# Performance work log

Measured on AMD Instinct MI355X. Metric: run time of the kernel, lower is better.

Reference implementation:

```python
import jax, jax.numpy as jnp
import numpy as np

NEG_SLOPE = 0.2
EPS = 1e-5


def gatv2_conv(x, src, dst, Wl, Wr, att, bias, n_nodes):
    # x: [N, F_in]; Wl, Wr: [F_in, H*C]; att: [H, C]; bias: [C]
    H, C = att.shape
    xl = (x @ Wl).reshape(n_nodes, H, C)
    xr = (x @ Wr).reshape(n_nodes, H, C)
    # edge-wise GATv2 score: att . leaky_relu(xl[src] + xr[dst])
    xls = xl[src]                                   # [E, H, C]
    e = jax.nn.leaky_relu(xls + xr[dst], negative_slope=NEG_SLOPE)
    score = jnp.einsum('ehc,hc->eh', e, att)        # [E, H]
    # segment softmax over incoming edges of each dst node
    m = jax.ops.segment_max(score, dst, num_segments=n_nodes)
    expv = jnp.exp(score - m[dst])
    denom = jax.ops.segment_sum(expv, dst, num_segments=n_nodes)
    alpha = expv / denom[dst]                       # [E, H]
    out = jax.ops.segment_sum(xls * alpha[:, :, None], dst, num_segments=n_nodes)  # [N, H, C]
    return out.mean(axis=1) + bias                  # concat=False -> mean heads


def batchnorm(x, gamma, beta):
    mu = x.mean(axis=0)
    var = x.var(axis=0)
    return (x - mu) * jax.lax.rsqrt(var + EPS) * gamma + beta


def setup_inputs() -> dict:
    key = jax.random.key(0)
    ks = jax.random.split(key, 16)
    N, E = 50000, 400000
    F_in, Hd, H, Z = 32, 64, 4, 64

    def glorot(k, shape):
        fan_in, fan_out = shape[0], shape[-1]
        s = float(np.sqrt(6.0 / (fan_in + fan_out)))
        return jax.random.uniform(k, shape, jnp.float32, -s, s)

    return {
        'x': jax.random.normal(ks[0], (N, F_in), jnp.float32),
        'edge_index': jax.random.randint(ks[1], (2, E), 0, N, jnp.int64),
        'l': jax.random.uniform(ks[2], (N,), jnp.float32),
        'Wl1': glorot(ks[3], (F_in, H * Hd)),
        'Wr1': glorot(ks[4], (F_in, H * Hd)),
        'att1': glorot(ks[5], (H, Hd)),
        'b1': jnp.zeros((Hd,), jnp.float32),
        'g1': jnp.ones((Hd,), jnp.float32),
        'be1': jnp.zeros((Hd,), jnp.float32),
        'Wl2': glorot(ks[6], (Hd + 1, H * Hd)),
        'Wr2': glorot(ks[7], (Hd + 1, H * Hd)),
        'att2': glorot(ks[8], (H, Hd)),
        'b2': jnp.zeros((Hd,), jnp.float32),
        'g2': jnp.ones((Hd,), jnp.float32),
        'be2': jnp.zeros((Hd,), jnp.float32),
        'Wlin': glorot(ks[9], (Hd, 2 * Z)),
        'blin': jnp.zeros((2 * Z,), jnp.float32),
    }


def reference(x, edge_index, l, Wl1, Wr1, att1, b1, g1, be1,
              Wl2, Wr2, att2, b2, g2, be2, Wlin, blin):
    N = x.shape[0]
    loop = jnp.arange(N, dtype=edge_index.dtype)
    src = jnp.concatenate([edge_index[0], loop])  # add self-loops (PyG default)
    dst = jnp.concatenate([edge_index[1], loop])

    h = gatv2_conv(x, src, dst, Wl1, Wr1, att1, b1, N)
    h = jax.nn.relu(batchnorm(h, g1, be1))
    h = jnp.concatenate([h, l[:, None]], axis=-1)
    h = gatv2_conv(h, src, dst, Wl2, Wr2, att2, b2, N)
    h = jax.nn.relu(batchnorm(h, g2, be2))
    h = h @ Wlin + blin
    return h.mean(axis=0)  # [2*z_dim]
```

## Files before the change

### kernel.cpp

```cpp
#include <hip/hip_runtime.h>
#include <hip/hip_bf16.h>

typedef __hip_bfloat16 bf16;
typedef unsigned short u16;
typedef unsigned char u8;

#define NEG 0.2f
#define BN_EPS 1e-5f
#define SLOTS 64

typedef __attribute__((ext_vector_type(8))) short bfrag;
typedef __attribute__((ext_vector_type(4))) float ffrag;
typedef __attribute__((ext_vector_type(2))) float f32x2;

__device__ __forceinline__ float u2f(u16 u) { return __uint_as_float(((unsigned)u) << 16); }
__device__ __forceinline__ float lo2f(unsigned u) { return __uint_as_float(u << 16); }
__device__ __forceinline__ float hi2f(unsigned u) { return __uint_as_float(u & 0xffff0000u); }
__device__ __forceinline__ u16 f2b(float f) { bf16 t = __float2bfloat16(f); return *(u16*)&t; }
__device__ __forceinline__ float leaky(float x) { return fmaxf(x, NEG * x); }

__device__ __forceinline__ void prep_body(const float* __restrict__ Wl,
                                          const float* __restrict__ Wr,
                                          u16* __restrict__ Wbf, int K, int idx) {
    const int l = idx & 63, n = (idx >> 6) & 31, s = idx >> 11;
    const int col = n * 16 + (l & 15);
    const int kbase = s * 32 + ((l >> 4) << 3);
    const float* __restrict__ W = (col < 256) ? (Wl + col) : (Wr + col - 256);
    u16 v[8];
    #pragma unroll
    for (int j = 0; j < 8; ++j) {
        const int k = kbase + j;
        v[j] = (k < K) ? f2b(W[(size_t)k * 256]) : (u16)0;
    }
    ushort4* d = reinterpret_cast<ushort4*>(Wbf + (size_t)idx * 8);
    d[0] = make_ushort4(v[0], v[1], v[2], v[3]);
    d[1] = make_ushort4(v[4], v[5], v[6], v[7]);
}

__global__ __launch_bounds__(256) void k_misc(
    const float* __restrict__ Wl1, const float* __restrict__ Wr1,
    const float* __restrict__ Wl2, const float* __restrict__ Wr2,
    u16* __restrict__ WbfA, u16* __restrict__ WbfB,
    const int* __restrict__ src, const int* __restrict__ dst,
    int* __restrict__ deg, int* __restrict__ csr_off, int E) {
    const int b = blockIdx.x;
    if (b < 8) {
        prep_body(Wl1, Wr1, WbfA, 32, b * 256 + threadIdx.x);
    } else if (b < 32) {
        prep_body(Wl2, Wr2, WbfB, 65, (b - 8) * 256 + threadIdx.x);
    } else {
        for (int e = (b - 32) * 256 + (int)threadIdx.x; e < E; e += 1024 * 256) {
            const int d = dst[e];
            const int slot = atomicAdd(&deg[d], 1);
            if (slot < SLOTS) csr_off[d * SLOTS + slot] = src[e] * 256;
        }
    }
}

template <int KSTEPS, int STAGE, int SAW>
__device__ __forceinline__ void gemm_body(
    int bid,
    const float* __restrict__ Xf,
    const u16* __restrict__ hagg,
    const float* __restrict__ sums, const float* __restrict__ sumsq,
    const float* __restrict__ g, const float* __restrict__ be,
    const float* __restrict__ lf,
    const u16* __restrict__ Wbf,
    u8* __restrict__ xl, u8* __restrict__ xr, int N) {

    __shared__ u16 sA[32 * SAW];
    __shared__ u8 sC[32 * 512];
    __shared__ float ssc[64], ssh[64];

    const int tid = threadIdx.x;
    const int row0 = bid * 32;

    if (STAGE == 1) {
        if (tid < 64) {
            const float invN = 1.0f / (float)N;
            const float mu = sums[tid] * invN;
            const float var = sumsq[tid] * invN - mu * mu;
            const float sc = rsqrtf(var + BN_EPS) * g[tid];
            ssc[tid] = sc;
            ssh[tid] = be[tid] - mu * sc;
        }
        __syncthreads();
        for (int idx = tid; idx < 32 * 12; idx += 256) {
            const int r = idx / 12, c0 = (idx % 12) * 8;
            const int rr = row0 + r;
            u16 o[8] = {0, 0, 0, 0, 0, 0, 0, 0};
            if (rr < N) {
                if (c0 < 64) {
                    const uint4 hv = *reinterpret_cast<const uint4*>(hagg + (size_t)rr * 64 + c0);
                    const float f[8] = {lo2f(hv.x), hi2f(hv.x), lo2f(hv.y), hi2f(hv.y),
                                        lo2f(hv.z), hi2f(hv.z), lo2f(hv.w), hi2f(hv.w)};
                    #pragma unroll
                    for (int j = 0; j < 8; ++j)
                        o[j] = f2b(fmaxf(0.f, f[j] * ssc[c0 + j] + ssh[c0 + j]));
                } else if (c0 == 64) {
                    o[0] = f2b(lf[rr]);
                }
            }
            ushort4* d = reinterpret_cast<ushort4*>(&sA[r * SAW + c0]);
            d[0] = make_ushort4(o[0], o[1], o[2], o[3]);
            d[1] = make_ushort4(o[4], o[5], o[6], o[7]);
        }
    } else {
        for (int idx = tid; idx < 32 * 8; idx += 256) {
            const int r = idx >> 3, c4 = (idx & 7) * 4;
            const int rr = row0 + r;
            float4 v = make_float4(0.f, 0.f, 0.f, 0.f);
            if (rr < N) v = *reinterpret_cast<const float4*>(Xf + (size_t)rr * 32 + c4);
            *reinterpret_cast<ushort4*>(&sA[r * SAW + c4]) =
                make_ushort4(f2b(v.x), f2b(v.y), f2b(v.z), f2b(v.w));
        }
    }
    __syncthreads();

    const int w = tid >> 6, l = tid & 63;
    ffrag acc[2][8];
    #pragma unroll
    for (int m = 0; m < 2; ++m)
        #pragma unroll
        for (int n = 0; n < 8; ++n) acc[m][n] = ffrag{0.f, 0.f, 0.f, 0.f};

    #pragma unroll
    for (int s = 0; s < KSTEPS; ++s) {
        bfrag bf[8];
        #pragma unroll
        for (int n = 0; n < 8; ++n) {
            const int ntile = w * 8 + n;
            bf[n] = *reinterpret_cast<const bfrag*>(Wbf + ((size_t)(s * 32 + ntile) * 64 + l) * 8);
        }
        bfrag af[2];
        #pragma unroll
        for (int m = 0; m < 2; ++m) {
            const int off = (m * 16 + (l & 15)) * SAW + s * 32 + ((l >> 4) << 3);
            af[m] = *reinterpret_cast<const bfrag*>(&sA[off]);
        }
        #pragma unroll
        for (int n = 0; n < 8; ++n) {
            acc[0][n] = __builtin_amdgcn_mfma_f32_16x16x32_bf16(af[0], bf[n], acc[0][n], 0, 0, 0);
            acc[1][n] = __builtin_amdgcn_mfma_f32_16x16x32_bf16(af[1], bf[n], acc[1][n], 0, 0, 0);
        }
    }

    #pragma unroll
    for (int m = 0; m < 2; ++m)
        #pragma unroll
        for (int n = 0; n < 8; ++n) {
            const int col = w * 128 + n * 16 + (l & 15);
            const int rbase = m * 16 + ((l >> 4) << 2);
            unsigned w01 = __builtin_amdgcn_cvt_pk_fp8_f32(acc[m][n][0], acc[m][n][1], 0u, false);
            unsigned w23 = __builtin_amdgcn_cvt_pk_fp8_f32(acc[m][n][2], acc[m][n][3], 0u, false);
            sC[(rbase + 0) * 512 + col] = (u8)(w01 & 0xff);
            sC[(rbase + 1) * 512 + col] = (u8)((w01 >> 8) & 0xff);
            sC[(rbase + 2) * 512 + col] = (u8)(w23 & 0xff);
            sC[(rbase + 3) * 512 + col] = (u8)((w23 >> 8) & 0xff);
        }
    __syncthreads();

    for (int idx = tid; idx < 32 * 32; idx += 256) {
        const int r = idx >> 5, c16 = (idx & 31) * 16;
        const int rr = row0 + r;
        if (rr >= N) continue;
        const uint4 v = *reinterpret_cast<const uint4*>(&sC[r * 512 + c16]);
        if (c16 < 256)
            *reinterpret_cast<uint4*>(xl + (size_t)rr * 256 + c16) = v;
        else
            *reinterpret_cast<uint4*>(xr + (size_t)rr * 256 + (c16 - 256)) = v;
    }
}

__global__ __launch_bounds__(256) void k_gemm1(
    const float* __restrict__ Xf, const u16* __restrict__ WbfA,
    u8* __restrict__ xl, u8* __restrict__ xr, int N) {
    gemm_body<1, 0, 40>(blockIdx.x, Xf, nullptr, nullptr, nullptr, nullptr, nullptr,
                        nullptr, WbfA, xl, xr, N);
}

__global__ __launch_bounds__(256) void k_gemm2(
    const u16* __restrict__ hagg,
    const float* __restrict__ sums, const float* __restrict__ sumsq,
    const float* __restrict__ g, const float* __restrict__ be,
    const float* __restrict__ lf, const u16* __restrict__ WbfB,
    u8* __restrict__ xl, u8* __restrict__ xr, int N) {
    gemm_body<3, 1, 104>(blockIdx.x, nullptr, hagg, sums, sumsq, g, be, lf, WbfB, xl, xr, N);
}

__global__ __launch_bounds__(256) void gat_fused(
    const u8* __restrict__ xl, const u8* __restrict__ xr,
    const int* __restrict__ csr_off, const int* __restrict__ deg,
    const float* __restrict__ att,
    u16* __restrict__ hagg, int N) {
    const int tid = threadIdx.x;
    const int wv = tid >> 6, lane = tid & 63;
    const int id = blockIdx.x * 4 + wv;
    if (id >= N) return;
    const int half = lane >> 5, hl = lane & 31;

    const float4 av0 = *reinterpret_cast<const float4*>(att + hl * 8);
    const float4 av1 = *reinterpret_cast<const float4*>(att + hl * 8 + 4);
    const char* xlb = (const char*)xl;
    const unsigned selfOff = (unsigned)id * 256u;
    const unsigned laneOff = (unsigned)hl * 8u;

    const uint2 bu = *reinterpret_cast<const uint2*>((const char*)xr + selfOff + laneOff);
    const f32x2 bu01 = __builtin_amdgcn_cvt_pk_f32_fp8(bu.x, false);
    const f32x2 bu23 = __builtin_amdgcn_cvt_pk_f32_fp8(bu.x, true);
    const f32x2 bu45 = __builtin_amdgcn_cvt_pk_f32_fp8(bu.y, false);
    const f32x2 bu67 = __builtin_amdgcn_cvt_pk_f32_fp8(bu.y, true);
    const float b0 = bu01.x, b1 = bu01.y, b2 = bu23.x, b3 = bu23.y;
    const float b4 = bu45.x, b5 = bu45.y, b6 = bu67.x, b7 = bu67.y;

    const int L = min(deg[id], SLOTS);

    unsigned idxA = selfOff;
    if (lane < L) idxA = (unsigned)csr_off[id * SLOTS + lane];

    auto offv = [&](int vi) -> unsigned {
        const unsigned o = (unsigned)__shfl((int)idxA, vi - 1);
        return (vi == 0) ? selfOff : o;
    };
    auto ldrow = [&](int vi) -> uint2 {
        return *reinterpret_cast<const uint2*>(xlb + (size_t)(offv(vi) + laneOff));
    };

    float ax0 = 0.f, ax1 = 0.f, ax2 = 0.f, ax3 = 0.f;
    float ax4 = 0.f, ax5 = 0.f, ax6 = 0.f, ax7 = 0.f;
    float denom = 0.f;

    uint2 A = ldrow(half);
    uint2 B = ldrow(2 + half);

    #define PROC(a, vi)                                                         \
    {                                                                           \
        const f32x2 u01 = __builtin_amdgcn_cvt_pk_f32_fp8((a).x, false);        \
        const f32x2 u23 = __builtin_amdgcn_cvt_pk_f32_fp8((a).x, true);         \
        const f32x2 u45 = __builtin_amdgcn_cvt_pk_f32_fp8((a).y, false);        \
        const f32x2 u67 = __builtin_amdgcn_cvt_pk_f32_fp8((a).y, true);         \
        const float x0 = u01.x, x1 = u01.y, x2 = u23.x, x3 = u23.y;             \
        const float x4 = u45.x, x5 = u45.y, x6 = u67.x, x7 = u67.y;             \
        float p = av0.x * leaky(x0 + b0) + av0.y * leaky(x1 + b1)               \
                + av0.z * leaky(x2 + b2) + av0.w * leaky(x3 + b3)               \
                + av1.x * leaky(x4 + b4) + av1.y * leaky(x5 + b5)               \
                + av1.z * leaky(x6 + b6) + av1.w * leaky(x7 + b7);              \
        p += __shfl_xor(p, 1);                                                  \
        p += __shfl_xor(p, 2);                                                  \
        p += __shfl_xor(p, 4);                                                  \
        const float ev = ((vi) <= L) ? __expf(p) : 0.f;                         \
        denom += ev;                                                            \
        ax0 += ev * x0; ax1 += ev * x1; ax2 += ev * x2; ax3 += ev * x3;         \
        ax4 += ev * x4; ax5 += ev * x5; ax6 += ev * x6; ax7 += ev * x7;         \
    }

    for (int ib = 0; ib <= L; ib += 4) {
        uint2 An = A, Bn = B;
        if (ib + 4 <= L) An = ldrow(ib + 4 + half);
        if (ib + 6 <= L) Bn = ldrow(ib + 6 + half);
        PROC(A, ib + half)
        PROC(B, ib + 2 + half)
        A = An; B = Bn;
    }
    #undef PROC

    denom += __shfl_xor(denom, 32);
    const float s = 0.25f / denom;
    float r0 = ax0 * s, r1 = ax1 * s, r2 = ax2 * s, r3 = ax3 * s;
    float r4 = ax4 * s, r5 = ax5 * s, r6 = ax6 * s, r7 = ax7 * s;

    #define RED(r) r += __shfl_xor(r, 8); r += __shfl_xor(r, 16); r += __shfl_xor(r, 32);
    RED(r0) RED(r1) RED(r2) RED(r3) RED(r4) RED(r5) RED(r6) RED(r7)
    #undef RED

    if (lane < 8) {
        union { u16 h[8]; uint4 v; } pk;
        pk.h[0] = f2b(r0); pk.h[1] = f2b(r1); pk.h[2] = f2b(r2); pk.h[3] = f2b(r3);
        pk.h[4] = f2b(r4); pk.h[5] = f2b(r5); pk.h[6] = f2b(r6); pk.h[7] = f2b(r7);
        *reinterpret_cast<uint4*>(hagg + (size_t)id * 64 + lane * 8) = pk.v;
    }
}

__global__ __launch_bounds__(256) void bn_stats(const u16* __restrict__ hagg,
                                                float* __restrict__ sums,
                                                float* __restrict__ sumsq, int N) {
    __shared__ float bsum[64], bsq[64];
    const int tid = threadIdx.x;
    if (tid < 64) { bsum[tid] = 0.f; bsq[tid] = 0.f; }
    __syncthreads();
    const int r0 = tid >> 3, cg = tid & 7;
    float s[8] = {0, 0, 0, 0, 0, 0, 0, 0}, q[8] = {0, 0, 0, 0, 0, 0, 0, 0};
    for (int n = blockIdx.x * 32 + r0; n < N; n += gridDim.x * 32) {
        const uint4 v = *reinterpret_cast<const uint4*>(hagg + (size_t)n * 64 + cg * 8);
        const float f[8] = {lo2f(v.x), hi2f(v.x), lo2f(v.y), hi2f(v.y),
                            lo2f(v.z), hi2f(v.z), lo2f(v.w), hi2f(v.w)};
        #pragma unroll
        for (int j = 0; j < 8; ++j) { s[j] += f[j]; q[j] += f[j] * f[j]; }
    }
    #pragma unroll
    for (int j = 0; j < 8; ++j) {
        atomicAdd(&bsum[cg * 8 + j], s[j]);
        atomicAdd(&bsq[cg * 8 + j], q[j]);
    }
    __syncthreads();
    if (tid < 64) {
        atomicAdd(&sums[tid], bsum[tid]);
        atomicAdd(&sumsq[tid], bsq[tid]);
    }
}

__global__ __launch_bounds__(256) void bnz_final(
    const u16* __restrict__ hagg,
    const float* __restrict__ sums, const float* __restrict__ sumsq,
    const float* __restrict__ g, const float* __restrict__ be,
    const float* __restrict__ Wlin, const float* __restrict__ blin,
    float* __restrict__ zbar, int* __restrict__ counter,
    float* __restrict__ out, int N) {
    __shared__ float ls[4][64];
    __shared__ float zb[64];
    __shared__ int lastFlag;
    const int tid = threadIdx.x;
    const int c = tid & 63, r = tid >> 6;
    const float invN = 1.0f / (float)N;
    const float mu = sums[c] * invN;
    const float var = sumsq[c] * invN - mu * mu;
    const float sc = rsqrtf(var + BN_EPS) * g[c];
    const float sh = be[c] - mu * sc;
    float s = 0.f;
    for (int n = blockIdx.x * 4 + r; n < N; n += gridDim.x * 4)
        s += fmaxf(0.f, u2f(hagg[(size_t)n * 64 + c]) * sc + sh);
    ls[r][c] = s;
    __syncthreads();
    if (tid < 64) {
        atomicAdd(&zbar[tid], ls[0][tid] + ls[1][tid] + ls[2][tid] + ls[3][tid]);
        __threadfence();
    }
    __syncthreads();
    if (tid == 0) lastFlag = (atomicAdd(counter, 1) == (int)gridDim.x - 1) ? 1 : 0;
    __syncthreads();
    if (lastFlag) {
        if (tid < 64) zb[tid] = atomicAdd(&zbar[tid], 0.0f);
        __syncthreads();
        if (tid < 128) {
            float acc = blin[tid];
            #pragma unroll 4
            for (int k = 0; k < 64; ++k) acc += (zb[k] * invN) * Wlin[(size_t)k * 128 + tid];
            out[tid] = acc;
        }
    }
}

static inline char* align16(char* p) {
    return (char*)(((uintptr_t)p + 15) & ~(uintptr_t)15);
}

extern "C" void kernel_launch(void* const* d_in, const int* in_sizes, int n_in,
                              void* d_out, int out_size, void* d_ws, size_t ws_size,
                              hipStream_t stream) {
    const float* x    = (const float*)d_in[0];
    const int*   ei   = (const int*)d_in[1];
    const float* l    = (const float*)d_in[2];
    const float* Wl1  = (const float*)d_in[3];
    const float* Wr1  = (const float*)d_in[4];
    const float* att1 = (const float*)d_in[5];
    const float* g1   = (const float*)d_in[7];
    const float* be1  = (const float*)d_in[8];
    const float* Wl2  = (const float*)d_in[9];
    const float* Wr2  = (const float*)d_in[10];
    const float* att2 = (const float*)d_in[11];
    const float* g2   = (const float*)d_in[13];
    const float* be2  = (const float*)d_in[14];
    const float* Wlin = (const float*)d_in[15];
    const float* blin = (const float*)d_in[16];
    float* out = (float*)d_out;

    const int N = in_sizes[2];
    const int E = in_sizes[1] / 2;
    const int* src = ei;
    const int* dst = ei + E;

    char* p = (char*)d_ws;
    u8* xl = (u8*)p;            p += (size_t)N * 256 * sizeof(u8);
    u8* xr = (u8*)p;            p += (size_t)N * 256 * sizeof(u8);
    u16* hagg = (u16*)p;        p += (size_t)N * 64 * sizeof(u16);  p = align16(p);
    u16* WbfA = (u16*)p;        p += (size_t)2048 * 8 * sizeof(u16);
    u16* WbfB = (u16*)p;        p += (size_t)6144 * 8 * sizeof(u16);
    int* csr_off = (int*)p;     p += (size_t)N * SLOTS * sizeof(int);  p = align16(p);
    char* zero0 = p;
    int* deg = (int*)p;         p += (size_t)N * sizeof(int);
    int* scalars = (int*)p;
    float* sums1 = (float*)p;   p += 64 * sizeof(float);
    float* sumsq1 = (float*)p;  p += 64 * sizeof(float);
    float* sums2 = (float*)p;   p += 64 * sizeof(float);
    float* sumsq2 = (float*)p;  p += 64 * sizeof(float);
    float* zbar = (float*)p;    p += 64 * sizeof(float);
    int* counter = (int*)p;     p += 192 * sizeof(int);
    const size_t zbytes = (size_t)(p - zero0);
    (void)scalars;

    const int gemmBlocks = (N + 31) / 32;
    const int nodeBlocks = (N + 3) / 4;

    hipMemsetAsync(zero0, 0, zbytes, stream);
    k_misc<<<32 + 1024, 256, 0, stream>>>(Wl1, Wr1, Wl2, Wr2, WbfA, WbfB,
                                          src, dst, deg, csr_off, E);
    k_gemm1<<<gemmBlocks, 256, 0, stream>>>(x, WbfA, xl, xr, N);
    gat_fused<<<nodeBlocks, 256, 0, stream>>>(xl, xr, csr_off, deg, att1, hagg, N);
    bn_stats<<<256, 256, 0, stream>>>(hagg, sums1, sumsq1, N);
    k_gemm2<<<gemmBlocks, 256, 0, stream>>>(hagg, sums1, sumsq1, g1, be1, l, WbfB, xl, xr, N);
    gat_fused<<<nodeBlocks, 256, 0, stream>>>(xl, xr, csr_off, deg, att2, hagg, N);
    bn_stats<<<256, 256, 0, stream>>>(hagg, sums2, sumsq2, N);
    bnz_final<<<256, 256, 0, stream>>>(hagg, sums2, sumsq2, g2, be2, Wlin, blin,
                                       zbar, counter, out, N);
}
```

Before: 188.2 us.

## Overlap edge scatter with first GEMM and pack GAT math into float2 ops

Moves the edge-to-CSR atomic scatter out of the weight-prep kernel and into extra blocks of the first GEMM launch, so the scatter runs alongside the projection GEMM and the small prep kernel stays short. It also rewrites the per-edge leaky-relu, attention dot product and accumulation in gat_fused using 2-wide float vectors, so the compiler can emit packed FP32 instructions. The packed form changes the summation order of the attention dot product slightly. The GEMM blocks now share the GPU with atomic-heavy scatter blocks, which may contend for memory bandwidth.

```diff
diff --git a/kernel.cpp b/kernel.cpp
--- a/kernel.cpp
+++ b/kernel.cpp
@@ -17,7 +17,6 @@
 __device__ __forceinline__ float lo2f(unsigned u) { return __uint_as_float(u << 16); }
 __device__ __forceinline__ float hi2f(unsigned u) { return __uint_as_float(u & 0xffff0000u); }
 __device__ __forceinline__ u16 f2b(float f) { bf16 t = __float2bfloat16(f); return *(u16*)&t; }
-__device__ __forceinline__ float leaky(float x) { return fmaxf(x, NEG * x); }
 
 __device__ __forceinline__ void prep_body(const float* __restrict__ Wl,
                                           const float* __restrict__ Wr,
@@ -37,24 +36,13 @@
     d[1] = make_ushort4(v[4], v[5], v[6], v[7]);
 }
 
-__global__ __launch_bounds__(256) void k_misc(
+__global__ __launch_bounds__(256) void k_prep(
     const float* __restrict__ Wl1, const float* __restrict__ Wr1,
     const float* __restrict__ Wl2, const float* __restrict__ Wr2,
-    u16* __restrict__ WbfA, u16* __restrict__ WbfB,
-    const int* __restrict__ src, const int* __restrict__ dst,
-    int* __restrict__ deg, int* __restrict__ csr_off, int E) {
+    u16* __restrict__ WbfA, u16* __restrict__ WbfB) {
     const int b = blockIdx.x;
-    if (b < 8) {
-        prep_body(Wl1, Wr1, WbfA, 32, b * 256 + threadIdx.x);
-    } else if (b < 32) {
-        prep_body(Wl2, Wr2, WbfB, 65, (b - 8) * 256 + threadIdx.x);
-    } else {
-        for (int e = (b - 32) * 256 + (int)threadIdx.x; e < E; e += 1024 * 256) {
-            const int d = dst[e];
-            const int slot = atomicAdd(&deg[d], 1);
-            if (slot < SLOTS) csr_off[d * SLOTS + slot] = src[e] * 256;
-        }
-    }
+    if (b < 8) prep_body(Wl1, Wr1, WbfA, 32, b * 256 + threadIdx.x);
+    else       prep_body(Wl2, Wr2, WbfB, 65, (b - 8) * 256 + threadIdx.x);
 }
 
 template <int KSTEPS, int STAGE, int SAW>
@@ -172,11 +160,22 @@
     }
 }
 
-__global__ __launch_bounds__(256) void k_gemm1(
+__global__ __launch_bounds__(256) void k_gemm1_scatter(
     const float* __restrict__ Xf, const u16* __restrict__ WbfA,
-    u8* __restrict__ xl, u8* __restrict__ xr, int N) {
-    gemm_body<1, 0, 40>(blockIdx.x, Xf, nullptr, nullptr, nullptr, nullptr, nullptr,
-                        nullptr, WbfA, xl, xr, N);
+    u8* __restrict__ xl, u8* __restrict__ xr, int N, int gemmBlocks,
+    const int* __restrict__ src, const int* __restrict__ dst,
+    int* __restrict__ deg, int* __restrict__ csr_off, int E) {
+    if ((int)blockIdx.x < gemmBlocks) {
+        gemm_body<1, 0, 40>(blockIdx.x, Xf, nullptr, nullptr, nullptr, nullptr, nullptr,
+                            nullptr, WbfA, xl, xr, N);
+    } else {
+        for (int e = ((int)blockIdx.x - gemmBlocks) * 256 + (int)threadIdx.x; e < E;
+             e += 1024 * 256) {
+            const int d = dst[e];
+            const int slot = atomicAdd(&deg[d], 1);
+            if (slot < SLOTS) csr_off[d * SLOTS + slot] = src[e] * 256;
+        }
+    }
 }
 
 __global__ __launch_bounds__(256) void k_gemm2(
@@ -199,19 +198,20 @@
     if (id >= N) return;
     const int half = lane >> 5, hl = lane & 31;
 
-    const float4 av0 = *reinterpret_cast<const float4*>(att + hl * 8);
-    const float4 av1 = *reinterpret_cast<const float4*>(att + hl * 8 + 4);
+    const f32x2 av01 = *reinterpret_cast<const f32x2*>(att + hl * 8);
+    const f32x2 av23 = *reinterpret_cast<const f32x2*>(att + hl * 8 + 2);
+    const f32x2 av45 = *reinterpret_cast<const f32x2*>(att + hl * 8 + 4);
+    const f32x2 av67 = *reinterpret_cast<const f32x2*>(att + hl * 8 + 6);
     const char* xlb = (const char*)xl;
     const unsigned selfOff = (unsigned)id * 256u;
     const unsigned laneOff = (unsigned)hl * 8u;
+    const f32x2 negv = {NEG, NEG};
 
     const uint2 bu = *reinterpret_cast<const uint2*>((const char*)xr + selfOff + laneOff);
-    const f32x2 bu01 = __builtin_amdgcn_cvt_pk_f32_fp8(bu.x, false);
-    const f32x2 bu23 = __builtin_amdgcn_cvt_pk_f32_fp8(bu.x, true);
-    const f32x2 bu45 = __builtin_amdgcn_cvt_pk_f32_fp8(bu.y, false);
-    const f32x2 bu67 = __builtin_amdgcn_cvt_pk_f32_fp8(bu.y, true);
-    const float b0 = bu01.x, b1 = bu01.y, b2 = bu23.x, b3 = bu23.y;
-    const float b4 = bu45.x, b5 = bu45.y, b6 = bu67.x, b7 = bu67.y;
+    const f32x2 b01 = __builtin_amdgcn_cvt_pk_f32_fp8(bu.x, false);
+    const f32x2 b23 = __builtin_amdgcn_cvt_pk_f32_fp8(bu.x, true);
+    const f32x2 b45 = __builtin_amdgcn_cvt_pk_f32_fp8(bu.y, false);
+    const f32x2 b67 = __builtin_amdgcn_cvt_pk_f32_fp8(bu.y, true);
 
     const int L = min(deg[id], SLOTS);
 
@@ -226,8 +226,7 @@
         return *reinterpret_cast<const uint2*>(xlb + (size_t)(offv(vi) + laneOff));
     };
 
-    float ax0 = 0.f, ax1 = 0.f, ax2 = 0.f, ax3 = 0.f;
-    float ax4 = 0.f, ax5 = 0.f, ax6 = 0.f, ax7 = 0.f;
+    f32x2 ax01 = {0.f, 0.f}, ax23 = {0.f, 0.f}, ax45 = {0.f, 0.f}, ax67 = {0.f, 0.f};
     float denom = 0.f;
 
     uint2 A = ldrow(half);
@@ -235,23 +234,29 @@
 
     #define PROC(a, vi)                                                         \
     {                                                                           \
-        const f32x2 u01 = __builtin_amdgcn_cvt_pk_f32_fp8((a).x, false);        \
-        const f32x2 u23 = __builtin_amdgcn_cvt_pk_f32_fp8((a).x, true);         \
-        const f32x2 u45 = __builtin_amdgcn_cvt_pk_f32_fp8((a).y, false);        \
-        const f32x2 u67 = __builtin_amdgcn_cvt_pk_f32_fp8((a).y, true);         \
-        const float x0 = u01.x, x1 = u01.y, x2 = u23.x, x3 = u23.y;             \
-        const float x4 = u45.x, x5 = u45.y, x6 = u67.x, x7 = u67.y;             \
-        float p = av0.x * leaky(x0 + b0) + av0.y * leaky(x1 + b1)               \
-                + av0.z * leaky(x2 + b2) + av0.w * leaky(x3 + b3)               \
-                + av1.x * leaky(x4 + b4) + av1.y * leaky(x5 + b5)               \
-                + av1.z * leaky(x6 + b6) + av1.w * leaky(x7 + b7);              \
+        const f32x2 x01 = __builtin_amdgcn_cvt_pk_f32_fp8((a).x, false);        \
+        const f32x2 x23 = __builtin_amdgcn_cvt_pk_f32_fp8((a).x, true);         \
+        const f32x2 x45 = __builtin_amdgcn_cvt_pk_f32_fp8((a).y, false);        \
+        const f32x2 x67 = __builtin_amdgcn_cvt_pk_f32_fp8((a).y, true);         \
+        const f32x2 s01 = x01 + b01, s23 = x23 + b23;                           \
+        const f32x2 s45 = x45 + b45, s67 = x67 + b67;                           \
+        const f32x2 l01 = __builtin_elementwise_max(s01, s01 * negv);           \
+        const f32x2 l23 = __builtin_elementwise_max(s23, s23 * negv);           \
+        const f32x2 l45 = __builtin_elementwise_max(s45, s45 * negv);           \
+        const f32x2 l67 = __builtin_elementwise_max(s67, s67 * negv);           \
+        f32x2 p2 = av01 * l01;                                                  \
+        p2 += av23 * l23;                                                       \
+        p2 += av45 * l45;                                                       \
+        p2 += av67 * l67;                                                       \
+        float p = p2.x + p2.y;                                                  \
         p += __shfl_xor(p, 1);                                                  \
         p += __shfl_xor(p, 2);                                                  \
         p += __shfl_xor(p, 4);                                                  \
         const float ev = ((vi) <= L) ? __expf(p) : 0.f;                         \
+        const f32x2 ev2 = {ev, ev};                                             \
         denom += ev;                                                            \
-        ax0 += ev * x0; ax1 += ev * x1; ax2 += ev * x2; ax3 += ev * x3;         \
-        ax4 += ev * x4; ax5 += ev * x5; ax6 += ev * x6; ax7 += ev * x7;         \
+        ax01 += ev2 * x01; ax23 += ev2 * x23;                                   \
+        ax45 += ev2 * x45; ax67 += ev2 * x67;                                   \
     }
 
     for (int ib = 0; ib <= L; ib += 4) {
@@ -266,8 +271,8 @@
 
     denom += __shfl_xor(denom, 32);
     const float s = 0.25f / denom;
-    float r0 = ax0 * s, r1 = ax1 * s, r2 = ax2 * s, r3 = ax3 * s;
-    float r4 = ax4 * s, r5 = ax5 * s, r6 = ax6 * s, r7 = ax7 * s;
+    float r0 = ax01.x * s, r1 = ax01.y * s, r2 = ax23.x * s, r3 = ax23.y * s;
+    float r4 = ax45.x * s, r5 = ax45.y * s, r6 = ax67.x * s, r7 = ax67.y * s;
 
     #define RED(r) r += __shfl_xor(r, 8); r += __shfl_xor(r, 16); r += __shfl_xor(r, 32);
     RED(r0) RED(r1) RED(r2) RED(r3) RED(r4) RED(r5) RED(r6) RED(r7)
@@ -388,7 +393,6 @@
     int* csr_off = (int*)p;     p += (size_t)N * SLOTS * sizeof(int);  p = align16(p);
     char* zero0 = p;
     int* deg = (int*)p;         p += (size_t)N * sizeof(int);
-    int* scalars = (int*)p;
     float* sums1 = (float*)p;   p += 64 * sizeof(float);
     float* sumsq1 = (float*)p;  p += 64 * sizeof(float);
     float* sums2 = (float*)p;   p += 64 * sizeof(float);
@@ -396,15 +400,14 @@
     float* zbar = (float*)p;    p += 64 * sizeof(float);
     int* counter = (int*)p;     p += 192 * sizeof(int);
     const size_t zbytes = (size_t)(p - zero0);
-    (void)scalars;
 
     const int gemmBlocks = (N + 31) / 32;
     const int nodeBlocks = (N + 3) / 4;
 
     hipMemsetAsync(zero0, 0, zbytes, stream);
-    k_misc<<<32 + 1024, 256, 0, stream>>>(Wl1, Wr1, Wl2, Wr2, WbfA, WbfB,
-                                          src, dst, deg, csr_off, E);
-    k_gemm1<<<gemmBlocks, 256, 0, stream>>>(x, WbfA, xl, xr, N);
+    k_prep<<<32, 256, 0, stream>>>(Wl1, Wr1, Wl2, Wr2, WbfA, WbfB);
+    k_gemm1_scatter<<<gemmBlocks + 1024, 256, 0, stream>>>(x, WbfA, xl, xr, N, gemmBlocks,
+                                                           src, dst, deg, csr_off, E);
     gat_fused<<<nodeBlocks, 256, 0, stream>>>(xl, xr, csr_off, deg, att1, hagg, N);
     bn_stats<<<256, 256, 0, stream>>>(hagg, sums1, sumsq1, N);
     k_gemm2<<<gemmBlocks, 256, 0, stream>>>(hagg, sums1, sumsq1, g1, be1, l, WbfB, xl, xr, N);
```

Measured after the change: 195.6 us. 1.04x slower.
